# Kernel optimization log

Measured on AMD Instinct MI355X. Metric: run time of the kernel, lower is better.

## Reference

```python
import jax, jax.numpy as jnp
import numpy as np
from jax import lax

B, S, D = 4, 128, 256
POOL = 3


def conv_block(x, w, b, stride, pool_k):
    # x: (N, Cin, H, W), w: (Cout, Cin, kh, kw)
    y = lax.conv_general_dilated(
        x, w, window_strides=(stride, stride), padding='VALID',
        dimension_numbers=('NCHW', 'OIHW', 'NCHW'))
    y = y + b[None, :, None, None]
    y = jax.nn.gelu(y, approximate=False)  # torch GELU default is exact
    # MaxPool2d(kernel_size=pool_k) -> stride = pool_k, VALID
    y = lax.reduce_window(y, -jnp.inf, lax.max,
                          (1, 1, pool_k, pool_k), (1, 1, pool_k, pool_k), 'VALID')
    return y


def setup_inputs() -> dict:
    key = jax.random.key(0)
    ks = jax.random.split(key, 8)
    token_features = jax.random.normal(ks[0], (B, S, D), dtype=jnp.float32)
    type_embedds = jax.random.normal(ks[1], (B, S, D), dtype=jnp.float32)
    # Conv2dFeatures(depth=3, num_channels=16, start_kernel=3, start_stride=2, pool_kernel=3)
    w1 = jax.random.normal(ks[2], (16, 1, 3, 3), dtype=jnp.float32) * 0.1
    b1 = jax.random.normal(ks[3], (16,), dtype=jnp.float32) * 0.01
    w2 = jax.random.normal(ks[4], (32, 16, 3, 3), dtype=jnp.float32) * 0.05
    b2 = jax.random.normal(ks[5], (32,), dtype=jnp.float32) * 0.01
    w3 = jax.random.normal(ks[6], (32, 32, 3, 3), dtype=jnp.float32) * 0.05
    b3 = jax.random.normal(ks[7], (32,), dtype=jnp.float32) * 0.01
    return dict(token_features=token_features, type_embedds=type_embedds,
                w1=w1, b1=b1, w2=w2, b2=b2, w3=w3, b3=b3)


def reference(token_features, type_embedds, w1, b1, w2, b2, w3, b3):
    b, s, d = type_embedds.shape
    # Outter2dFusion: fused[n,s,i,j] = type_embedds[n,s,i] * token_features[n,s,j]
    fused = jnp.einsum('bsi,bsj->bsij', type_embedds, token_features)
    # Conv stack applied per seq position with in_channels=1 == one batched conv
    x = fused.reshape(b * s, 1, d, d)
    x = conv_block(x, w1, b1, stride=2, pool_k=POOL)
    x = conv_block(x, w2, b2, stride=1, pool_k=POOL)
    x = conv_block(x, w3, b3, stride=1, pool_k=POOL)
    # Dropout is identity in eval mode
    return x.reshape(b, s, -1)
```

## Files before the change

kernel.cpp:

```cpp
#include <hip/hip_runtime.h>
#include <math.h>


#define NIMG 512

__device__ __forceinline__ float gelu_exact(float x) {
    return 0.5f * x * (1.0f + erff(x * 0.70710678118654752f));
}
__device__ __forceinline__ float pool_gelu(float vmin, float vmax) {
    return fmaxf(gelu_exact(vmin), gelu_exact(vmax));
}

typedef __attribute__((address_space(3))) char lds_char;
typedef const __attribute__((address_space(1))) char glb_char;
__device__ __forceinline__ void gl_lds16(const void* g, void* l) {
    __builtin_amdgcn_global_load_lds((glb_char*)g, (lds_char*)l, 16, 0, 0);
}

__global__ __launch_bounds__(256) void k1_fused(const float* __restrict__ tok,
                                                const float* __restrict__ typ,
                                                const float* __restrict__ w1,
                                                const float* __restrict__ b1,
                                                float* __restrict__ s1) {
    const int blk = blockIdx.x;
    const int img = blk >> 1;
    const int py0 = (blk & 1) * 21;
    const int tid = threadIdx.x;
    const int c     = tid >> 4;
    const int pslot = tid & 15;

    float wv[9];
#pragma unroll
    for (int k = 0; k < 9; ++k) wv[k] = w1[c * 9 + k];
    const float bias = b1[c];

    const float* frow = tok + img * 256;
    const float* trow = typ + img * 256;

    float g[3][3][3];
    int pxv[3];
#pragma unroll
    for (int s = 0; s < 3; ++s) {
        const int px = pslot + 16 * s;
        pxv[s] = px;
        const int pe = px < 42 ? px : 41;
        float f7[7];
#pragma unroll
        for (int q = 0; q < 7; ++q) f7[q] = frow[6 * pe + q];
#pragma unroll
        for (int di = 0; di < 3; ++di)
#pragma unroll
            for (int wx = 0; wx < 3; ++wx)
                g[s][di][wx] = wv[di * 3 + 0] * f7[2 * wx]
                             + wv[di * 3 + 1] * f7[2 * wx + 1]
                             + wv[di * 3 + 2] * f7[2 * wx + 2];
    }

    float* orow = s1 + ((size_t)img * 16 + c) * (42 * 44);
    for (int py = py0; py < py0 + 21; ++py) {
        float ts[7];
#pragma unroll
        for (int q = 0; q < 7; ++q) ts[q] = trow[6 * py + q];
#pragma unroll
        for (int s = 0; s < 3; ++s) {
            float vmin = INFINITY, vmax = -INFINITY;
#pragma unroll
            for (int wy = 0; wy < 3; ++wy) {
#pragma unroll
                for (int wx = 0; wx < 3; ++wx) {
                    float v = ts[2 * wy] * g[s][0][wx];
                    v = fmaf(ts[2 * wy + 1], g[s][1][wx], v);
                    v = fmaf(ts[2 * wy + 2], g[s][2][wx], v);
                    vmin = fminf(vmin, v);
                    vmax = fmaxf(vmax, v);
                }
            }
            if (pxv[s] < 42)
                orow[py * 44 + pxv[s]] = pool_gelu(vmin + bias, vmax + bias);
        }
    }
}

__global__ __launch_bounds__(256) void k2_conv(const float* __restrict__ s1,
                                               const float* __restrict__ w2,
                                               const float* __restrict__ b2,
                                               float* __restrict__ s2) {
    const int blk = blockIdx.x;
    const int img = blk >> 1;
    const int cog = blk & 1;
    __shared__ float4 slab4[2][512];

    const int tid  = threadIdx.x;
    const int lane = tid & 63;
    const int grp  = tid >> 6;
    const int wbase64 = tid & ~63;

    int base[3], valid[3], py[3], px[3];
#pragma unroll
    for (int tI = 0; tI < 3; ++tI) {
        const int cc0 = lane + 64 * tI;
        valid[tI] = (cc0 < 169);
        const int cc = valid[tI] ? cc0 : 168;
        py[tI] = cc / 13;
        px[tI] = cc % 13;
        base[tI] = py[tI] * 132 + px[tI] * 3;
    }

    float acc[4][3][9];
#pragma unroll
    for (int a = 0; a < 4; ++a)
#pragma unroll
        for (int tI = 0; tI < 3; ++tI)
#pragma unroll
            for (int k = 0; k < 9; ++k) acc[a][tI][k] = 0.f;

    const float* s1img = s1 + (size_t)img * 16 * 1848;

    {
        const char* src = (const char*)(s1img);
        gl_lds16(src + (size_t)tid * 16,        (char*)&slab4[0][0] + (size_t)wbase64 * 16);
        gl_lds16(src + (size_t)(256 + tid) * 16,(char*)&slab4[0][256] + (size_t)wbase64 * 16);
    }
    asm volatile("s_waitcnt vmcnt(0)" ::: "memory");
    __syncthreads();

#pragma unroll 1
    for (int cin = 0; cin < 16; ++cin) {
        const int cur = cin & 1;
        if (cin < 15) {
            const char* src = (const char*)(s1img + (cin + 1) * 1848);
            gl_lds16(src + (size_t)tid * 16,         (char*)&slab4[cur ^ 1][0] + (size_t)wbase64 * 16);
            gl_lds16(src + (size_t)(256 + tid) * 16, (char*)&slab4[cur ^ 1][256] + (size_t)wbase64 * 16);
        }

        const int wb = __builtin_amdgcn_readfirstlane((cog * 16 + grp) * 144 + cin * 9);
        float wv[4][9];
#pragma unroll
        for (int a = 0; a < 4; ++a)
#pragma unroll
            for (int k = 0; k < 9; ++k) wv[a][k] = w2[wb + a * 576 + k];

        const float* slab = (const float*)&slab4[cur][0];
#pragma unroll
        for (int tI = 0; tI < 3; ++tI) {
            float win[5][5];
#pragma unroll
            for (int r = 0; r < 5; ++r)
#pragma unroll
                for (int c2 = 0; c2 < 5; ++c2)
                    win[r][c2] = slab[base[tI] + r * 44 + c2];
#pragma unroll
            for (int wy = 0; wy < 3; ++wy)
#pragma unroll
                for (int wx = 0; wx < 3; ++wx)
#pragma unroll
                    for (int dy = 0; dy < 3; ++dy)
#pragma unroll
                        for (int dx = 0; dx < 3; ++dx) {
                            const float v = win[wy + dy][wx + dx];
#pragma unroll
                            for (int a = 0; a < 4; ++a)
                                acc[a][tI][wy * 3 + wx] =
                                    fmaf(v, wv[a][dy * 3 + dx], acc[a][tI][wy * 3 + wx]);
                        }
        }

        asm volatile("s_waitcnt vmcnt(0)" ::: "memory");
        __syncthreads();
    }

#pragma unroll
    for (int tI = 0; tI < 3; ++tI) {
        if (valid[tI]) {
#pragma unroll
            for (int a = 0; a < 4; ++a) {
                float vmin = INFINITY, vmax = -INFINITY;
#pragma unroll
                for (int k = 0; k < 9; ++k) {
                    vmin = fminf(vmin, acc[a][tI][k]);
                    vmax = fmaxf(vmax, acc[a][tI][k]);
                }
                const int co = cog * 16 + grp + 4 * a;
                const float b = b2[co];
                s2[((img * 32 + co) * 13 + py[tI]) * 13 + px[tI]] =
                    pool_gelu(vmin + b, vmax + b);
            }
        }
    }
}

__global__ __launch_bounds__(192) void k3_conv(const float* __restrict__ s2,
                                               const float* __restrict__ w3,
                                               const float* __restrict__ b3,
                                               float* __restrict__ out) {
    const int img = blockIdx.x;
    __shared__ float4 s2l4[1352];
    __shared__ float wl[32 * 32 * 9];
    float* s2l = (float*)s2l4;

    const int tid = threadIdx.x;
    const float4* src = (const float4*)(s2 + (size_t)img * 5408);
    for (int i = tid; i < 1352; i += 192) s2l4[i] = src[i];
    for (int i = tid; i < 9216; i += 192) wl[i] = w3[i];
    __syncthreads();

    if (tid < 144) {
        const int cp   = tid / 9;
        const int cell = tid % 9;
        const int cy = cell / 3, cx = cell % 3;
        const int base = (3 * cy) * 13 + 3 * cx;
        const int co0 = 2 * cp, co1 = 2 * cp + 1;

        float acc[2][9];
#pragma unroll
        for (int a = 0; a < 2; ++a)
#pragma unroll
            for (int k = 0; k < 9; ++k) acc[a][k] = 0.f;

        for (int cin = 0; cin < 32; ++cin) {
            float win[5][5];
#pragma unroll
            for (int r = 0; r < 5; ++r)
#pragma unroll
                for (int c2 = 0; c2 < 5; ++c2)
                    win[r][c2] = s2l[cin * 169 + base + r * 13 + c2];
            float wk[2][9];
#pragma unroll
            for (int k = 0; k < 9; ++k) {
                wk[0][k] = wl[(co0 * 32 + cin) * 9 + k];
                wk[1][k] = wl[(co1 * 32 + cin) * 9 + k];
            }
#pragma unroll
            for (int wy = 0; wy < 3; ++wy)
#pragma unroll
                for (int wx = 0; wx < 3; ++wx)
#pragma unroll
                    for (int dy = 0; dy < 3; ++dy)
#pragma unroll
                        for (int dx = 0; dx < 3; ++dx) {
                            const float v = win[wy + dy][wx + dx];
                            acc[0][wy * 3 + wx] = fmaf(v, wk[0][dy * 3 + dx], acc[0][wy * 3 + wx]);
                            acc[1][wy * 3 + wx] = fmaf(v, wk[1][dy * 3 + dx], acc[1][wy * 3 + wx]);
                        }
        }

#pragma unroll
        for (int a = 0; a < 2; ++a) {
            float vmin = INFINITY, vmax = -INFINITY;
#pragma unroll
            for (int k = 0; k < 9; ++k) {
                vmin = fminf(vmin, acc[a][k]);
                vmax = fmaxf(vmax, acc[a][k]);
            }
            const int co = a ? co1 : co0;
            const float b = b3[co];
            out[(size_t)img * 288 + co * 9 + cell] = pool_gelu(vmin + b, vmax + b);
        }
    }
}

extern "C" void kernel_launch(void* const* d_in, const int* in_sizes, int n_in,
                              void* d_out, int out_size, void* d_ws, size_t ws_size,
                              hipStream_t stream) {
    const float* tok = (const float*)d_in[0];
    const float* typ = (const float*)d_in[1];
    const float* w1  = (const float*)d_in[2];
    const float* b1  = (const float*)d_in[3];
    const float* w2  = (const float*)d_in[4];
    const float* b2  = (const float*)d_in[5];
    const float* w3  = (const float*)d_in[6];
    const float* b3  = (const float*)d_in[7];
    float* out = (float*)d_out;

    float* s1 = (float*)d_ws;
    float* s2 = s1 + (size_t)NIMG * 16 * 42 * 44;

    k1_fused<<<dim3(NIMG * 2), dim3(256), 0, stream>>>(tok, typ, w1, b1, s1);
    k2_conv<<<dim3(NIMG * 2), dim3(256), 0, stream>>>(s1, w2, b2, s2);
    k3_conv<<<dim3(NIMG), dim3(192), 0, stream>>>(s2, w3, b3, out);
}
```

Measured before the change: 254.4 us.

## Triple-buffer conv2 input slabs and read conv3 inputs directly from global

In the second conv kernel, the double-buffered LDS slab becomes a three-deep ring. Loads are issued two channels ahead and synchronised with a partial vmcnt wait plus one barrier per iteration, replacing the wait and barrier at the end of each iteration. The aim is to hide global-to-LDS latency behind compute. In the third conv kernel, the LDS staging of the image activations is removed and windows are read straight from global memory through the cache, which saves the staging copy and LDS space but adds uncached-risk global loads inside the channel loop.

```diff
diff --git a/kernel.cpp b/kernel.cpp
--- a/kernel.cpp
+++ b/kernel.cpp
@@ -88,7 +88,7 @@
     const int blk = blockIdx.x;
     const int img = blk >> 1;
     const int cog = blk & 1;
-    __shared__ float4 slab4[2][512];
+    __shared__ float4 slab4[3][512];
 
     const int tid  = threadIdx.x;
     const int lane = tid & 63;
@@ -116,21 +116,25 @@
 
     const float* s1img = s1 + (size_t)img * 16 * 1848;
 
-    {
-        const char* src = (const char*)(s1img);
-        gl_lds16(src + (size_t)tid * 16,        (char*)&slab4[0][0] + (size_t)wbase64 * 16);
-        gl_lds16(src + (size_t)(256 + tid) * 16,(char*)&slab4[0][256] + (size_t)wbase64 * 16);
-    }
-    asm volatile("s_waitcnt vmcnt(0)" ::: "memory");
-    __syncthreads();
+#pragma unroll
+    for (int p = 0; p < 2; ++p) {
+        const char* src = (const char*)(s1img + p * 1848);
+        gl_lds16(src + (size_t)tid * 16,         (char*)&slab4[p][0] + (size_t)wbase64 * 16);
+        gl_lds16(src + (size_t)(256 + tid) * 16, (char*)&slab4[p][256] + (size_t)wbase64 * 16);
+    }
 
 #pragma unroll 1
     for (int cin = 0; cin < 16; ++cin) {
-        const int cur = cin & 1;
-        if (cin < 15) {
-            const char* src = (const char*)(s1img + (cin + 1) * 1848);
-            gl_lds16(src + (size_t)tid * 16,         (char*)&slab4[cur ^ 1][0] + (size_t)wbase64 * 16);
-            gl_lds16(src + (size_t)(256 + tid) * 16, (char*)&slab4[cur ^ 1][256] + (size_t)wbase64 * 16);
+        const int cur = cin % 3;
+        if (cin != 15) asm volatile("s_waitcnt vmcnt(2)" ::: "memory");
+        else           asm volatile("s_waitcnt vmcnt(0)" ::: "memory");
+        __builtin_amdgcn_s_barrier();
+
+        if (cin + 2 < 16) {
+            const int nb = (cin + 2) % 3;
+            const char* src = (const char*)(s1img + (cin + 2) * 1848);
+            gl_lds16(src + (size_t)tid * 16,         (char*)&slab4[nb][0] + (size_t)wbase64 * 16);
+            gl_lds16(src + (size_t)(256 + tid) * 16, (char*)&slab4[nb][256] + (size_t)wbase64 * 16);
         }
 
         const int wb = __builtin_amdgcn_readfirstlane((cog * 16 + grp) * 144 + cin * 9);
@@ -164,9 +168,6 @@
                                     fmaf(v, wv[a][dy * 3 + dx], acc[a][tI][wy * 3 + wx]);
                         }
         }
-
-        asm volatile("s_waitcnt vmcnt(0)" ::: "memory");
-        __syncthreads();
     }
 
 #pragma unroll
@@ -194,13 +195,9 @@
                                                const float* __restrict__ b3,
                                                float* __restrict__ out) {
     const int img = blockIdx.x;
-    __shared__ float4 s2l4[1352];
     __shared__ float wl[32 * 32 * 9];
-    float* s2l = (float*)s2l4;
 
     const int tid = threadIdx.x;
-    const float4* src = (const float4*)(s2 + (size_t)img * 5408);
-    for (int i = tid; i < 1352; i += 192) s2l4[i] = src[i];
     for (int i = tid; i < 9216; i += 192) wl[i] = w3[i];
     __syncthreads();
 
@@ -210,6 +207,7 @@
         const int cy = cell / 3, cx = cell % 3;
         const int base = (3 * cy) * 13 + 3 * cx;
         const int co0 = 2 * cp, co1 = 2 * cp + 1;
+        const float* s2img = s2 + (size_t)img * 5408 + base;
 
         float acc[2][9];
 #pragma unroll
@@ -217,13 +215,15 @@
 #pragma unroll
             for (int k = 0; k < 9; ++k) acc[a][k] = 0.f;
 
+#pragma unroll 1
         for (int cin = 0; cin < 32; ++cin) {
+            const float* sl = s2img + cin * 169;
             float win[5][5];
 #pragma unroll
             for (int r = 0; r < 5; ++r)
 #pragma unroll
                 for (int c2 = 0; c2 < 5; ++c2)
-                    win[r][c2] = s2l[cin * 169 + base + r * 13 + c2];
+                    win[r][c2] = sl[r * 13 + c2];
             float wk[2][9];
 #pragma unroll
             for (int k = 0; k < 9; ++k) {
```

After: 254.7 us. About the same (+0.1%).
